# Kernel optimization log

Measured on AMD Instinct MI355X. Metric: run time of the kernel, lower is better.

## Reference

```python
import jax, jax.numpy as jnp
import numpy as np

VOCAB = 4096
CODE_DIM = 3
DECAY = 0.99
EPS = 1e-05
BETA = 0.25


def setup_inputs() -> dict:
    key = jax.random.key(0)
    k1, k2, k3, k4 = jax.random.split(key, 4)
    B, L, D = 4, 16384, CODE_DIM
    feats = jax.random.normal(k1, (B, L, D), dtype=jnp.float32)
    embed = jax.random.normal(k2, (VOCAB, D), dtype=jnp.float32) * 0.02  # trunc_normal std=init_gain
    ema_cluster_size = jax.random.uniform(k3, (VOCAB,), dtype=jnp.float32)
    ema_weight = jax.random.normal(k4, (VOCAB, D), dtype=jnp.float32) * 0.02
    return {"feats": feats, "embed": embed,
            "ema_cluster_size": ema_cluster_size, "ema_weight": ema_weight}


def reference(feats, embed, ema_cluster_size, ema_weight):
    B, L, D = feats.shape
    V = embed.shape[0]
    flat = feats.reshape(-1, D)  # (N, D)

    # squared-distance argmin nearest-codebook lookup
    dist = (jnp.sum(flat * flat, axis=1, keepdims=True)
            - 2.0 * flat @ embed.T
            + jnp.sum(embed * embed, axis=1))
    idx = jnp.argmin(dist, axis=1)  # (N,)

    quant = embed[idx].reshape(B, L, D)

    # VQ losses (embedding is frozen in torch; stop_grad for faithful grads)
    e_latent_loss = jnp.mean((quant - jax.lax.stop_gradient(feats)) ** 2)
    commit_loss = BETA * jnp.mean((feats - jax.lax.stop_gradient(quant)) ** 2)
    vq_loss = e_latent_loss + commit_loss

    # EMA codebook update (training branch): scatter-accumulate per code
    ones = jnp.ones_like(idx, dtype=flat.dtype)
    batch_cluster_size = jax.ops.segment_sum(ones, idx, num_segments=V)        # == one_hot.sum(0)
    batch_weight_sum = jax.ops.segment_sum(flat, idx, num_segments=V)          # == one_hot.T @ flat

    new_cluster_size = DECAY * ema_cluster_size + (1.0 - DECAY) * batch_cluster_size
    new_ema_weight = DECAY * ema_weight + (1.0 - DECAY) * batch_weight_sum

    n = jnp.sum(new_cluster_size)
    cluster_size = (new_cluster_size + EPS) / (n + V * EPS) * n
    new_embed = new_ema_weight / cluster_size[:, None]

    # code_dim == 3: renormalize the (cos, sin) columns to unit norm
    cos_sin = new_embed[:, 1:]
    norm = jnp.maximum(jnp.linalg.norm(cos_sin, axis=1, keepdims=True), EPS)
    new_embed = jnp.concatenate([new_embed[:, :1], cos_sin / norm], axis=1)

    # straight-through estimator
    quant_st = feats + jax.lax.stop_gradient(quant - feats)

    return (quant_st, idx.reshape(B, L), vq_loss,
            new_embed, new_cluster_size, new_ema_weight)
```

## Files before the change

kernel.cpp:

```cpp
#include <hip/hip_runtime.h>
#include <math.h>

#define VOCAB 4096
#define NROWS 65536
#define DECAYF 0.99f
#define EPSF 1e-5f

typedef unsigned long long u64;
typedef unsigned int u32;
typedef float vf2 __attribute__((ext_vector_type(2)));

static __device__ __forceinline__ vf2 pk_mul(vf2 a, vf2 b) {
    vf2 d; asm("v_pk_mul_f32 %0, %1, %2" : "=v"(d) : "v"(a), "v"(b)); return d;
}
static __device__ __forceinline__ vf2 pk_add(vf2 a, vf2 b) {
    vf2 d; asm("v_pk_add_f32 %0, %1, %2" : "=v"(d) : "v"(a), "v"(b)); return d;
}
static __device__ __forceinline__ vf2 pk_fma(vf2 a, vf2 b, vf2 c) {
    vf2 d; asm("v_pk_fma_f32 %0, %1, %2, %3" : "=v"(d) : "v"(a), "v"(b), "v"(c)); return d;
}
static __device__ __forceinline__ float min3f(float a, float b, float c) {
    float d; asm("v_min3_f32 %0, %1, %2, %3" : "=v"(d) : "v"(a), "v"(b), "v"(c)); return d;
}


__global__ __launch_bounds__(1024, 4) void vq_scan_kernel(
    const float* __restrict__ feats,
    const float* __restrict__ embed,
    float* __restrict__ quant_out,
    float* __restrict__ idx_out,
    double* __restrict__ errpart) {
    #pragma clang fp contract(off)
    __shared__ float4 tab[VOCAB];

    const int tid  = threadIdx.x;
    const int wave = tid >> 6;
    const int lane = tid & 63;

    #pragma unroll
    for (int k = 0; k < 2; ++k) {
        const int p = tid + k * 1024;
        const float* e = embed + p * 6;
        const float x0 = e[0], y0 = e[1], z0 = e[2];
        const float x1 = e[3], y1 = e[4], z1 = e[5];
        const float s0 = (x0 * x0 + y0 * y0) + z0 * z0;
        const float s1 = (x1 * x1 + y1 * y1) + z1 * z1;
        tab[2 * p]     = make_float4(-2.f * x0, -2.f * x1, -2.f * y0, -2.f * y1);
        tab[2 * p + 1] = make_float4(-2.f * z0, -2.f * z1, s0, s1);
    }

    const int rbase = blockIdx.x * 256 + lane * 4;
    const float4 fa = *(const float4*)(feats + rbase * 3);
    const float4 fb = *(const float4*)(feats + rbase * 3 + 4);
    const float4 fc = *(const float4*)(feats + rbase * 3 + 8);
    const float f0[4] = {fa.x, fa.w, fb.z, fc.y};
    const float f1[4] = {fa.y, fb.x, fb.w, fc.z};
    const float f2[4] = {fa.z, fb.y, fc.x, fc.w};
    vf2 f0s[4], f1s[4], f2s[4], fss[4];
    #pragma unroll
    for (int r = 0; r < 4; ++r) {
        const float fs = (f0[r] * f0[r] + f1[r] * f1[r]) + f2[r] * f2[r];
        f0s[r] = (vf2){f0[r], f0[r]};
        f1s[r] = (vf2){f1[r], f1[r]};
        f2s[r] = (vf2){f2[r], f2[r]};
        fss[r] = (vf2){fs, fs};
    }

    __syncthreads();

    float best[4] = {INFINITY, INFINITY, INFINITY, INFINITY};
    int   gb[4]   = {0, 0, 0, 0};
    const float4* __restrict__ wt = tab + (wave << 8);
    const int cw = wave << 8;

    for (int g = 0; g < 32; ++g) {
        const float4 A0 = wt[8 * g + 0], B0 = wt[8 * g + 1];
        const float4 A1 = wt[8 * g + 2], B1 = wt[8 * g + 3];
        const float4 A2 = wt[8 * g + 4], B2 = wt[8 * g + 5];
        const float4 A3 = wt[8 * g + 6], B3 = wt[8 * g + 7];
        const vf2 xs0 = {A0.x, A0.y}, ys0 = {A0.z, A0.w}, zs0 = {B0.x, B0.y}, es0 = {B0.z, B0.w};
        const vf2 xs1 = {A1.x, A1.y}, ys1 = {A1.z, A1.w}, zs1 = {B1.x, B1.y}, es1 = {B1.z, B1.w};
        const vf2 xs2 = {A2.x, A2.y}, ys2 = {A2.z, A2.w}, zs2 = {B2.x, B2.y}, es2 = {B2.z, B2.w};
        const vf2 xs3 = {A3.x, A3.y}, ys3 = {A3.z, A3.w}, zs3 = {B3.x, B3.y}, es3 = {B3.z, B3.w};
        const int cbase = cw + (g << 3);
        #pragma unroll
        for (int r = 0; r < 4; ++r) {
            vf2 d0 = pk_add(pk_add(fss[r], pk_fma(zs0, f2s[r], pk_fma(ys0, f1s[r], pk_mul(xs0, f0s[r])))), es0);
            vf2 d1 = pk_add(pk_add(fss[r], pk_fma(zs1, f2s[r], pk_fma(ys1, f1s[r], pk_mul(xs1, f0s[r])))), es1);
            vf2 d2 = pk_add(pk_add(fss[r], pk_fma(zs2, f2s[r], pk_fma(ys2, f1s[r], pk_mul(xs2, f0s[r])))), es2);
            vf2 d3 = pk_add(pk_add(fss[r], pk_fma(zs3, f2s[r], pk_fma(ys3, f1s[r], pk_mul(xs3, f0s[r])))), es3);
            const float m1 = min3f(d0.x, d0.y, d1.x);
            const float m2 = min3f(d1.y, d2.x, d2.y);
            const float m3 = min3f(d3.x, d3.y, m1);
            const float m8 = fminf(m2, m3);
            if (m8 < best[r]) { best[r] = m8; gb[r] = cbase; }
        }
    }

    u64 key[4];
    #pragma unroll
    for (int r = 0; r < 4; ++r) {
        const int b0 = gb[r];
        const float bv = best[r];
        int idx = b0;
        #pragma unroll
        for (int k = 3; k >= 0; --k) {
            const float4 A = tab[b0 + 2 * k];
            const float4 B = tab[b0 + 2 * k + 1];
            const vf2 xs = {A.x, A.y}, ys = {A.z, A.w}, zs = {B.x, B.y}, es = {B.z, B.w};
            vf2 d = pk_add(pk_add(fss[r], pk_fma(zs, f2s[r], pk_fma(ys, f1s[r], pk_mul(xs, f0s[r])))), es);
            if (d.y == bv) idx = b0 + 2 * k + 1;
            if (d.x == bv) idx = b0 + 2 * k;
        }
        const u32 bb = __float_as_uint(bv);
        const u32 mb = bb ^ ((u32)((int)bb >> 31) | 0x80000000u);
        key[r] = ((u64)mb << 32) | (u32)idx;
    }

    __syncthreads();
    u64* mk = (u64*)tab;
    if (wave != 0) {
        #pragma unroll
        for (int r = 0; r < 4; ++r)
            mk[(wave * 4 + r) * 64 + lane] = key[r];
    }
    __syncthreads();
    if (wave == 0) {
        for (int w = 1; w < 16; ++w) {
            #pragma unroll
            for (int r = 0; r < 4; ++r) {
                const u64 k = mk[(w * 4 + r) * 64 + lane];
                key[r] = k < key[r] ? k : key[r];
            }
        }
        int cand[4];
        #pragma unroll
        for (int r = 0; r < 4; ++r) cand[r] = (int)(u32)key[r];

        *(float4*)(idx_out + rbase) =
            make_float4((float)cand[0], (float)cand[1], (float)cand[2], (float)cand[3]);

        float q[4][3];
        #pragma unroll
        for (int r = 0; r < 4; ++r) {
            q[r][0] = embed[cand[r] * 3 + 0];
            q[r][1] = embed[cand[r] * 3 + 1];
            q[r][2] = embed[cand[r] * 3 + 2];
        }
        *(float4*)(quant_out + rbase * 3)     = make_float4(q[0][0], q[0][1], q[0][2], q[1][0]);
        *(float4*)(quant_out + rbase * 3 + 4) = make_float4(q[1][1], q[1][2], q[2][0], q[2][1]);
        *(float4*)(quant_out + rbase * 3 + 8) = make_float4(q[2][2], q[3][0], q[3][1], q[3][2]);

        float err = 0.0f;
        #pragma unroll
        for (int r = 0; r < 4; ++r) {
            const float d0 = q[r][0] - f0[r], d1 = q[r][1] - f1[r], d2 = q[r][2] - f2[r];
            err += d0 * d0 + d1 * d1 + d2 * d2;
        }
        #pragma unroll
        for (int off = 32; off >= 1; off >>= 1) err += __shfl_xor(err, off);
        if (lane == 0) errpart[blockIdx.x] = (double)err;
    }
}

__global__ __launch_bounds__(1024) void seg_kernel(
    const float* __restrict__ feats,
    const float* __restrict__ idx_f,
    const float* __restrict__ ema_cs,
    float4* __restrict__ part,
    float* __restrict__ n_out,
    int iters, int nseg) {
    __shared__ float lcnt[VOCAB];
    __shared__ float lw[VOCAB * 3];
    const int t = threadIdx.x;
    const int b = blockIdx.x;

    if (b == nseg) {
        float s = ema_cs[t] + ema_cs[t + 1024] + ema_cs[t + 2048] + ema_cs[t + 3072];
        #pragma unroll
        for (int off = 32; off >= 1; off >>= 1) s += __shfl_xor(s, off);
        if ((t & 63) == 0) lcnt[t >> 6] = s;
        __syncthreads();
        if (t == 0) {
            float S = 0.f;
            #pragma unroll
            for (int w = 0; w < 16; ++w) S += lcnt[w];
            *n_out = DECAYF * S + (1.0f - DECAYF) * (float)NROWS;
        }
        return;
    }

    #pragma unroll
    for (int i = 0; i < 4; ++i)  lcnt[t + i * 1024] = 0.0f;
    #pragma unroll
    for (int i = 0; i < 12; ++i) lw[t + i * 1024] = 0.0f;
    __syncthreads();

    const int base = b * iters * 1024;
    for (int i = 0; i < iters; ++i) {
        const int row = base + i * 1024 + t;
        const int cand = (int)idx_f[row];
        atomicAdd(&lcnt[cand], 1.0f);
        atomicAdd(&lw[cand * 3 + 0], feats[row * 3 + 0]);
        atomicAdd(&lw[cand * 3 + 1], feats[row * 3 + 1]);
        atomicAdd(&lw[cand * 3 + 2], feats[row * 3 + 2]);
    }
    __syncthreads();

    #pragma unroll
    for (int i = 0; i < 4; ++i) {
        const int v = t + i * 1024;
        part[b * VOCAB + v] = make_float4(lcnt[v], lw[3 * v], lw[3 * v + 1], lw[3 * v + 2]);
    }
}

__global__ __launch_bounds__(256) void ema_final_kernel(
    const float4* __restrict__ part,
    const float* __restrict__ ema_cs,
    const float* __restrict__ ema_w,
    const double* __restrict__ errpart,
    const float* __restrict__ n_out,
    float* __restrict__ ncs_out,
    float* __restrict__ nw_out,
    float* __restrict__ embed_out,
    float* __restrict__ loss_out,
    int nseg) {
    const int v = blockIdx.x * 256 + threadIdx.x;
    float c = 0.f, w0 = 0.f, w1 = 0.f, w2 = 0.f;
    for (int b = 0; b < nseg; ++b) {
        const float4 p = part[b * VOCAB + v];
        c += p.x; w0 += p.y; w1 += p.z; w2 += p.w;
    }
    const float ncs = DECAYF * ema_cs[v] + (1.0f - DECAYF) * c;
    const float n0  = DECAYF * ema_w[v * 3 + 0] + (1.0f - DECAYF) * w0;
    const float n1  = DECAYF * ema_w[v * 3 + 1] + (1.0f - DECAYF) * w1;
    const float n2  = DECAYF * ema_w[v * 3 + 2] + (1.0f - DECAYF) * w2;
    ncs_out[v] = ncs;
    nw_out[v * 3 + 0] = n0;
    nw_out[v * 3 + 1] = n1;
    nw_out[v * 3 + 2] = n2;

    const float n = *n_out;
    const float cs = (ncs + EPSF) / (n + (float)VOCAB * EPSF) * n;
    const float d0 = n0 / cs;
    const float d1 = n1 / cs;
    const float d2 = n2 / cs;
    const float nrm = fmaxf(sqrtf(d1 * d1 + d2 * d2), EPSF);
    embed_out[v * 3 + 0] = d0;
    embed_out[v * 3 + 1] = d1 / nrm;
    embed_out[v * 3 + 2] = d2 / nrm;

    if (blockIdx.x == 0) {
        __shared__ double se[256];
        const int t = threadIdx.x;
        se[t] = errpart[t];
        __syncthreads();
        #pragma unroll
        for (int s = 128; s > 0; s >>= 1) {
            if (t < s) se[t] += se[t + s];
            __syncthreads();
        }
        if (t == 0)
            loss_out[0] = (float)(1.25 * se[0] / (double)(NROWS * 3));
    }
}

extern "C" void kernel_launch(void* const* d_in, const int* in_sizes, int n_in,
                              void* d_out, int out_size, void* d_ws, size_t ws_size,
                              hipStream_t stream) {
    const float* feats  = (const float*)d_in[0];
    const float* embed  = (const float*)d_in[1];
    const float* ema_cs = (const float*)d_in[2];
    const float* ema_w  = (const float*)d_in[3];

    float* out = (float*)d_out;
    float* quant_out = out;
    float* idx_out   = out + 196608;
    float* loss_out  = out + 262144;
    float* embed_out = out + 262145;
    float* ncs_out   = out + 274433;
    float* nw_out    = out + 278529;

    char* wsb = (char*)d_ws;
    double* errpart = (double*)wsb;
    float*  n_out   = (float*)(wsb + 2048);
    float4* part    = (float4*)(wsb + 4096);

    const size_t per_seg = (size_t)VOCAB * 16;
    const size_t avail = ws_size > 4096 ? ws_size - 4096 : 0;
    int nseg = 8;
    if (avail >= 64 * per_seg)      nseg = 64;
    else if (avail >= 32 * per_seg) nseg = 32;
    else if (avail >= 16 * per_seg) nseg = 16;
    const int iters = NROWS / (nseg * 1024);

    vq_scan_kernel<<<NROWS / 256, 1024, 0, stream>>>(feats, embed,
                                                     quant_out, idx_out, errpart);
    seg_kernel<<<nseg + 1, 1024, 0, stream>>>(feats, idx_out, ema_cs,
                                              part, n_out, iters, nseg);
    ema_final_kernel<<<VOCAB / 256, 256, 0, stream>>>(part, ema_cs, ema_w,
                                                      errpart, n_out,
                                                      ncs_out, nw_out, embed_out,
                                                      loss_out, nseg);
}
```

Measured before the change: 65.27 us.

## Split codebook scan across two blocks per row tile and fuse epilogue into segment kernel

```diff
diff --git a/kernel.cpp b/kernel.cpp
--- a/kernel.cpp
+++ b/kernel.cpp
@@ -24,32 +24,31 @@
 }
 
 
-__global__ __launch_bounds__(1024, 4) void vq_scan_kernel(
+__global__ __launch_bounds__(1024, 8) void vq_scan_kernel(
     const float* __restrict__ feats,
     const float* __restrict__ embed,
-    float* __restrict__ quant_out,
-    float* __restrict__ idx_out,
-    double* __restrict__ errpart) {
+    u64* __restrict__ keys) {
     #pragma clang fp contract(off)
-    __shared__ float4 tab[VOCAB];
+    __shared__ float4 tab[2048];
 
     const int tid  = threadIdx.x;
     const int wave = tid >> 6;
     const int lane = tid & 63;
-
-    #pragma unroll
-    for (int k = 0; k < 2; ++k) {
-        const int p = tid + k * 1024;
-        const float* e = embed + p * 6;
+    const int rblk = blockIdx.x >> 1;
+    const int half = blockIdx.x & 1;
+    const int cbase = half << 11;
+
+    {
+        const float* e = embed + (cbase + 2 * tid) * 3;
         const float x0 = e[0], y0 = e[1], z0 = e[2];
         const float x1 = e[3], y1 = e[4], z1 = e[5];
         const float s0 = (x0 * x0 + y0 * y0) + z0 * z0;
         const float s1 = (x1 * x1 + y1 * y1) + z1 * z1;
-        tab[2 * p]     = make_float4(-2.f * x0, -2.f * x1, -2.f * y0, -2.f * y1);
-        tab[2 * p + 1] = make_float4(-2.f * z0, -2.f * z1, s0, s1);
-    }
-
-    const int rbase = blockIdx.x * 256 + lane * 4;
+        tab[2 * tid]     = make_float4(-2.f * x0, -2.f * x1, -2.f * y0, -2.f * y1);
+        tab[2 * tid + 1] = make_float4(-2.f * z0, -2.f * z1, s0, s1);
+    }
+
+    const int rbase = rblk * 256 + lane * 4;
     const float4 fa = *(const float4*)(feats + rbase * 3);
     const float4 fb = *(const float4*)(feats + rbase * 3 + 4);
     const float4 fc = *(const float4*)(feats + rbase * 3 + 8);
@@ -70,10 +69,10 @@
 
     float best[4] = {INFINITY, INFINITY, INFINITY, INFINITY};
     int   gb[4]   = {0, 0, 0, 0};
-    const float4* __restrict__ wt = tab + (wave << 8);
-    const int cw = wave << 8;
-
-    for (int g = 0; g < 32; ++g) {
+    const float4* __restrict__ wt = tab + (wave << 7);
+    const int cw = wave << 7;
+
+    for (int g = 0; g < 16; ++g) {
         const float4 A0 = wt[8 * g + 0], B0 = wt[8 * g + 1];
         const float4 A1 = wt[8 * g + 2], B1 = wt[8 * g + 3];
         const float4 A2 = wt[8 * g + 4], B2 = wt[8 * g + 5];
@@ -82,7 +81,7 @@
         const vf2 xs1 = {A1.x, A1.y}, ys1 = {A1.z, A1.w}, zs1 = {B1.x, B1.y}, es1 = {B1.z, B1.w};
         const vf2 xs2 = {A2.x, A2.y}, ys2 = {A2.z, A2.w}, zs2 = {B2.x, B2.y}, es2 = {B2.z, B2.w};
         const vf2 xs3 = {A3.x, A3.y}, ys3 = {A3.z, A3.w}, zs3 = {B3.x, B3.y}, es3 = {B3.z, B3.w};
-        const int cbase = cw + (g << 3);
+        const int lbase = cw + (g << 3);
         #pragma unroll
         for (int r = 0; r < 4; ++r) {
             vf2 d0 = pk_add(pk_add(fss[r], pk_fma(zs0, f2s[r], pk_fma(ys0, f1s[r], pk_mul(xs0, f0s[r])))), es0);
@@ -93,7 +92,7 @@
             const float m2 = min3f(d1.y, d2.x, d2.y);
             const float m3 = min3f(d3.x, d3.y, m1);
             const float m8 = fminf(m2, m3);
-            if (m8 < best[r]) { best[r] = m8; gb[r] = cbase; }
+            if (m8 < best[r]) { best[r] = m8; gb[r] = lbase; }
         }
     }
 
@@ -114,7 +113,7 @@
         }
         const u32 bb = __float_as_uint(bv);
         const u32 mb = bb ^ ((u32)((int)bb >> 31) | 0x80000000u);
-        key[r] = ((u64)mb << 32) | (u32)idx;
+        key[r] = ((u64)mb << 32) | (u32)(cbase + idx);
     }
 
     __syncthreads();
@@ -133,43 +132,24 @@
                 key[r] = k < key[r] ? k : key[r];
             }
         }
-        int cand[4];
-        #pragma unroll
-        for (int r = 0; r < 4; ++r) cand[r] = (int)(u32)key[r];
-
-        *(float4*)(idx_out + rbase) =
-            make_float4((float)cand[0], (float)cand[1], (float)cand[2], (float)cand[3]);
-
-        float q[4][3];
-        #pragma unroll
-        for (int r = 0; r < 4; ++r) {
-            q[r][0] = embed[cand[r] * 3 + 0];
-            q[r][1] = embed[cand[r] * 3 + 1];
-            q[r][2] = embed[cand[r] * 3 + 2];
-        }
-        *(float4*)(quant_out + rbase * 3)     = make_float4(q[0][0], q[0][1], q[0][2], q[1][0]);
-        *(float4*)(quant_out + rbase * 3 + 4) = make_float4(q[1][1], q[1][2], q[2][0], q[2][1]);
-        *(float4*)(quant_out + rbase * 3 + 8) = make_float4(q[2][2], q[3][0], q[3][1], q[3][2]);
-
-        float err = 0.0f;
-        #pragma unroll
-        for (int r = 0; r < 4; ++r) {
-            const float d0 = q[r][0] - f0[r], d1 = q[r][1] - f1[r], d2 = q[r][2] - f2[r];
-            err += d0 * d0 + d1 * d1 + d2 * d2;
-        }
-        #pragma unroll
-        for (int off = 32; off >= 1; off >>= 1) err += __shfl_xor(err, off);
-        if (lane == 0) errpart[blockIdx.x] = (double)err;
+        u64* kh = keys + half * NROWS;
+        #pragma unroll
+        for (int r = 0; r < 4; ++r) kh[rbase + r] = key[r];
     }
 }
 
 __global__ __launch_bounds__(1024) void seg_kernel(
     const float* __restrict__ feats,
-    const float* __restrict__ idx_f,
+    const float* __restrict__ embed,
+    const u64* __restrict__ keys,
     const float* __restrict__ ema_cs,
+    float* __restrict__ quant_out,
+    float* __restrict__ idx_out,
     float4* __restrict__ part,
+    double* __restrict__ errpart,
     float* __restrict__ n_out,
     int iters, int nseg) {
+    #pragma clang fp contract(off)
     __shared__ float lcnt[VOCAB];
     __shared__ float lw[VOCAB * 3];
     const int t = threadIdx.x;
@@ -196,14 +176,32 @@
     for (int i = 0; i < 12; ++i) lw[t + i * 1024] = 0.0f;
     __syncthreads();
 
+    float err = 0.0f;
     const int base = b * iters * 1024;
     for (int i = 0; i < iters; ++i) {
         const int row = base + i * 1024 + t;
-        const int cand = (int)idx_f[row];
+        const u64 k0 = keys[row];
+        const u64 k1 = keys[row + NROWS];
+        const int cand = (int)(u32)(k0 < k1 ? k0 : k1);
+
+        const float fx = feats[row * 3 + 0];
+        const float fy = feats[row * 3 + 1];
+        const float fz = feats[row * 3 + 2];
+
+        idx_out[row] = (float)cand;
+        const float qx = embed[cand * 3 + 0];
+        const float qy = embed[cand * 3 + 1];
+        const float qz = embed[cand * 3 + 2];
+        quant_out[row * 3 + 0] = qx;
+        quant_out[row * 3 + 1] = qy;
+        quant_out[row * 3 + 2] = qz;
+        const float dx = qx - fx, dy = qy - fy, dz = qz - fz;
+        err += dx * dx + dy * dy + dz * dz;
+
         atomicAdd(&lcnt[cand], 1.0f);
-        atomicAdd(&lw[cand * 3 + 0], feats[row * 3 + 0]);
-        atomicAdd(&lw[cand * 3 + 1], feats[row * 3 + 1]);
-        atomicAdd(&lw[cand * 3 + 2], feats[row * 3 + 2]);
+        atomicAdd(&lw[cand * 3 + 0], fx);
+        atomicAdd(&lw[cand * 3 + 1], fy);
+        atomicAdd(&lw[cand * 3 + 2], fz);
     }
     __syncthreads();
 
@@ -211,6 +209,19 @@
     for (int i = 0; i < 4; ++i) {
         const int v = t + i * 1024;
         part[b * VOCAB + v] = make_float4(lcnt[v], lw[3 * v], lw[3 * v + 1], lw[3 * v + 2]);
+    }
+
+    __syncthreads();
+    #pragma unroll
+    for (int off = 32; off >= 1; off >>= 1) err += __shfl_xor(err, off);
+    double* ed = (double*)lcnt;
+    if ((t & 63) == 0) ed[t >> 6] = (double)err;
+    __syncthreads();
+    if (t == 0) {
+        double s = 0.0;
+        #pragma unroll
+        for (int w = 0; w < 16; ++w) s += ed[w];
+        errpart[b] = s;
     }
 }
 
@@ -253,7 +264,7 @@
     if (blockIdx.x == 0) {
         __shared__ double se[256];
         const int t = threadIdx.x;
-        se[t] = errpart[t];
+        se[t] = (t < nseg) ? errpart[t] : 0.0;
         __syncthreads();
         #pragma unroll
         for (int s = 128; s > 0; s >>= 1) {
@@ -284,20 +295,24 @@
     char* wsb = (char*)d_ws;
     double* errpart = (double*)wsb;
     float*  n_out   = (float*)(wsb + 2048);
-    float4* part    = (float4*)(wsb + 4096);
-
+    u64*    keys    = (u64*)(wsb + 4096);
+    float4* part    = (float4*)(wsb + 4096 + 2 * (size_t)NROWS * 8);
+
+    const size_t used = 4096 + 2 * (size_t)NROWS * 8;
     const size_t per_seg = (size_t)VOCAB * 16;
-    const size_t avail = ws_size > 4096 ? ws_size - 4096 : 0;
-    int nseg = 8;
+    const size_t avail = ws_size > used ? ws_size - used : 0;
+    int nseg = 2;
     if (avail >= 64 * per_seg)      nseg = 64;
     else if (avail >= 32 * per_seg) nseg = 32;
     else if (avail >= 16 * per_seg) nseg = 16;
+    else if (avail >= 8 * per_seg)  nseg = 8;
+    else if (avail >= 4 * per_seg)  nseg = 4;
     const int iters = NROWS / (nseg * 1024);
 
-    vq_scan_kernel<<<NROWS / 256, 1024, 0, stream>>>(feats, embed,
-                                                     quant_out, idx_out, errpart);
-    seg_kernel<<<nseg + 1, 1024, 0, stream>>>(feats, idx_out, ema_cs,
-                                              part, n_out, iters, nseg);
+    vq_scan_kernel<<<512, 1024, 0, stream>>>(feats, embed, keys);
+    seg_kernel<<<nseg + 1, 1024, 0, stream>>>(feats, embed, keys, ema_cs,
+                                              quant_out, idx_out, part,
+                                              errpart, n_out, iters, nseg);
     ema_final_kernel<<<VOCAB / 256, 256, 0, stream>>>(part, ema_cs, ema_w,
                                                       errpart, n_out,
                                                       ncs_out, nw_out, embed_out,
```

Measured after the change: 223.4 us. 3.42x slower.
